# Kernel optimization log

Measured on AMD Instinct MI355X. Metric: run time of the kernel, lower is better.

## Reference

```python
import jax, jax.numpy as jnp
import numpy as np

B, N, F_IN, F_OUT, E = 8, 20000, 128, 128, 320000
ALPHA = 0.2  # LeakyReLU negative slope


def _xavier_normal(key, shape, gain=1.414):
    fan_in, fan_out = shape[0], shape[1]
    std = gain * np.sqrt(2.0 / (fan_in + fan_out))
    return jax.random.normal(key, shape, dtype=jnp.float32) * std


def setup_inputs() -> dict:
    key = jax.random.key(0)
    k1, k2, k3, k4, k5 = jax.random.split(key, 5)
    x = jax.random.normal(k1, (B, N, F_IN), dtype=jnp.float32)
    W = _xavier_normal(k2, (F_IN, F_OUT))
    a = _xavier_normal(k3, (2 * F_OUT, 1))
    # Edge list (src, dst). First N src are arange so every row has >=1 edge
    # (avoids div-by-zero in rowsum, matching a graph with no isolated sources).
    src_extra = jax.random.randint(k4, (E - N,), 0, N, dtype=jnp.int32)
    src = jnp.concatenate([jnp.arange(N, dtype=jnp.int32), src_extra])
    dst = jax.random.randint(k5, (E,), 0, N, dtype=jnp.int32)
    edge = jnp.stack([src, dst], axis=0)  # [2, E]
    return {"x": x, "W": W, "a": a, "edge": edge}


def reference(x, W, a, edge):
    # x: [B, N, F_in], W: [F_in, F_out], a: [2*F_out, 1], edge: [2, E]
    Fo = W.shape[1]
    n = x.shape[1]
    src, dst = edge[0], edge[1]
    h = jnp.einsum('bnf,fo->bno', x, W)  # [B, N, Fo]
    # cat(h[src], h[dst]) @ a  ==  (h @ a1)[src] + (h @ a2)[dst]
    a1, a2 = a[:Fo, 0], a[Fo:, 0]
    s = (h @ a1)[:, src] + (h @ a2)[:, dst]  # [B, E]
    score = jnp.where(s > 0, s, ALPHA * s)  # LeakyReLU
    e = jnp.exp(-score)  # [B, E]
    # spmm: h_prime[src] += e * h[dst]; rowsum[src] += e  (per batch)
    msg = e[..., None] * h[:, dst, :]  # [B, E, Fo]
    seg = jax.vmap(lambda m: jax.ops.segment_sum(m, src, num_segments=n))(msg)  # [B,N,Fo]
    rowsum = jax.vmap(lambda v: jax.ops.segment_sum(v, src, num_segments=n))(e)  # [B,N]
    h_prime = seg / rowsum[..., None]
    return jax.nn.elu(h_prime)  # concat=True -> ELU
```

## Files before the change

kernel.cpp:

```cpp
#include <hip/hip_runtime.h>

#define NB 8
#define NN 20000
#define FI 128
#define FO 128
#define NE 320000
#define ROWS (NB * NN)
#define LRALPHA 0.2f

typedef short bf16x8 __attribute__((ext_vector_type(8)));
typedef float f32x4 __attribute__((ext_vector_type(4)));

static __device__ __forceinline__ float b2f(unsigned short u) {
  return __uint_as_float(((unsigned int)u) << 16);
}
static __device__ __forceinline__ unsigned short f2b(float f) {
  unsigned int u = __float_as_uint(f);
  return (unsigned short)((u + 0x7FFFu + ((u >> 16) & 1u)) >> 16);
}

__global__ __launch_bounds__(256) void wt_kernel(const float* __restrict__ W,
                                                 unsigned short* __restrict__ Wb,
                                                 int* __restrict__ counts) {
  int idx = blockIdx.x * 256 + threadIdx.x;
  if (idx < FI * FO) {
    int k = idx >> 7, o = idx & 127;
    Wb[o * 128 + k] = f2b(W[idx]);
  }
  if (idx < NN) counts[idx] = 0;
}

#define LDW 136

__global__ __launch_bounds__(256) void gemm_kernel(
    const float* __restrict__ x, const unsigned short* __restrict__ Wb,
    const float* __restrict__ a,
    unsigned short* __restrict__ hb,
    float* __restrict__ g1, float* __restrict__ g2) {
  __shared__ __align__(16) unsigned short Ws[128 * LDW];
  const int tid = threadIdx.x;

  {
    const bf16x8* wsrc = (const bf16x8*)Wb;
#pragma unroll
    for (int it = 0; it < 8; ++it) {
      int c = tid + it * 256;
      int o = c >> 4, seg = c & 15;
      *(bf16x8*)&Ws[o * LDW + seg * 8] = wsrc[c];
    }
  }

  const int wv = tid >> 6;
  const int lane = tid & 63;
  const int m = lane & 15;
  const int quad = lane >> 4;
  const size_t row0 = (size_t)blockIdx.x * 64 + wv * 16;

  const float* xr = x + (row0 + m) * 128;
  bf16x8 afr[4];
#pragma unroll
  for (int k0 = 0; k0 < 4; ++k0) {
    const float4* xp = (const float4*)(xr + k0 * 32 + quad * 8);
    float4 v0 = xp[0];
    float4 v1 = xp[1];
    union { bf16x8 v; unsigned short u[8]; } af;
    af.u[0] = f2b(v0.x); af.u[1] = f2b(v0.y);
    af.u[2] = f2b(v0.z); af.u[3] = f2b(v0.w);
    af.u[4] = f2b(v1.x); af.u[5] = f2b(v1.y);
    af.u[6] = f2b(v1.z); af.u[7] = f2b(v1.w);
    afr[k0] = af.v;
  }
  __syncthreads();

  f32x4 acc[8] = {};
#pragma unroll
  for (int k0 = 0; k0 < 4; ++k0) {
#pragma unroll
    for (int c = 0; c < 8; ++c) {
      bf16x8 bf = *(const bf16x8*)&Ws[(c * 16 + m) * LDW + k0 * 32 + quad * 8];
      acc[c] = __builtin_amdgcn_mfma_f32_16x16x32_bf16(afr[k0], bf, acc[c], 0, 0, 0);
    }
  }

  unsigned short* hp = hb + row0 * 128;
#pragma unroll
  for (int c = 0; c < 8; ++c)
#pragma unroll
    for (int r = 0; r < 4; ++r)
      hp[(quad * 4 + r) * 128 + c * 16 + m] = f2b(acc[c][r]);

  float a1v[8], a2v[8];
#pragma unroll
  for (int c = 0; c < 8; ++c) {
    a1v[c] = a[c * 16 + m];
    a2v[c] = a[128 + c * 16 + m];
  }
  float p1[4] = {}, p2[4] = {};
#pragma unroll
  for (int c = 0; c < 8; ++c)
#pragma unroll
    for (int r = 0; r < 4; ++r) {
      p1[r] = fmaf(acc[c][r], a1v[c], p1[r]);
      p2[r] = fmaf(acc[c][r], a2v[c], p2[r]);
    }
#pragma unroll
  for (int off = 1; off < 16; off <<= 1)
#pragma unroll
    for (int r = 0; r < 4; ++r) {
      p1[r] += __shfl_xor(p1[r], off, 64);
      p2[r] += __shfl_xor(p2[r], off, 64);
    }
  if (m == 0) {
    size_t rbase = row0 + quad * 4;
#pragma unroll
    for (int r = 0; r < 4; ++r) {
      g1[rbase + r] = p1[r];
      g2[rbase + r] = p2[r];
    }
  }
}

__global__ __launch_bounds__(256) void hist_kernel(const int* __restrict__ src,
                                                   int* __restrict__ counts) {
  int e = blockIdx.x * 256 + threadIdx.x;
  if (e < NE) atomicAdd(&counts[src[e]], 1);
}

__global__ __launch_bounds__(1024) void scan_kernel(
    const int* __restrict__ counts, int* __restrict__ offsets,
    int* __restrict__ cursor) {
  __shared__ int sc[NN];
  __shared__ int sums[1024];
  const int t = threadIdx.x;
  for (int idx = t; idx < NN; idx += 1024) sc[idx] = counts[idx];
  __syncthreads();
  int local[20];
  int base = t * 20;
  int s = 0;
#pragma unroll
  for (int c = 0; c < 20; ++c) {
    int idx = base + c;
    int v = (idx < NN) ? sc[idx] : 0;
    local[c] = s;
    s += v;
  }
  sums[t] = s;
  __syncthreads();
  for (int off = 1; off < 1024; off <<= 1) {
    int u = 0;
    if (t >= off) u = sums[t - off];
    __syncthreads();
    sums[t] += u;
    __syncthreads();
  }
  int prefix = sums[t] - s;
#pragma unroll
  for (int c = 0; c < 20; ++c) {
    int idx = base + c;
    if (idx < NN) {
      int o = prefix + local[c];
      offsets[idx] = o;
      cursor[idx] = o;
    }
  }
  if (t == 0) offsets[NN] = NE;
}

__global__ __launch_bounds__(256) void scatter_kernel(
    const int* __restrict__ src, const int* __restrict__ dst,
    int* __restrict__ cursor, int* __restrict__ csr_dst) {
  int e = blockIdx.x * 256 + threadIdx.x;
  if (e < NE) {
    int s = src[e];
    int d = dst[e];
    int pos = atomicAdd(&cursor[s], 1);
    csr_dst[pos] = d;
  }
}

__global__ __launch_bounds__(64) void gather_kernel(
    const unsigned short* __restrict__ hb, const float* __restrict__ g1,
    const float* __restrict__ g2, const int* __restrict__ offsets,
    const int* __restrict__ csr_dst, float* __restrict__ out) {
  const int i = blockIdx.x;
  const int b = blockIdx.y;
  const int lane = threadIdx.x;
  const int quad = lane >> 4;
  const int beg = offsets[i];
  const int deg = offsets[i + 1] - beg;
  const float g1i = g1[(size_t)b * NN + i];
  const float* g2b = g2 + (size_t)b * NN;
  const char* hbase = (const char*)(hb + (size_t)b * NN * 128) + (lane & 15) * 16;

  float acc[8] = {};
  float rs = 0.f;
  for (int c0 = 0; c0 < deg; c0 += 64) {
    const int cnt = min(64, deg - c0);
    int myd = 0;
    float w = 0.f;
    if (lane < cnt) {
      myd = csr_dst[beg + c0 + lane];
      float s = g1i + g2b[myd];
      float sc = fmaxf(s, LRALPHA * s);
      w = __expf(-sc);
    }
    rs += w;
    const int cr = (cnt + 15) & ~15;
    for (int e = 0; e < cr; e += 16) {
      bf16x8 hv[4];
      float we[4];
#pragma unroll
      for (int j = 0; j < 4; ++j) {
        int idx = e + j * 4 + quad;
        int d = __shfl(myd, idx, 64);
        we[j] = __shfl(w, idx, 64);
        hv[j] = *(const bf16x8*)(hbase + (d << 8));
      }
#pragma unroll
      for (int j = 0; j < 4; ++j) {
        union { bf16x8 v; unsigned short u[8]; } hu;
        hu.v = hv[j];
#pragma unroll
        for (int k = 0; k < 8; ++k)
          acc[k] = fmaf(we[j], b2f(hu.u[k]), acc[k]);
      }
    }
  }
#pragma unroll
  for (int k = 0; k < 8; ++k) {
    acc[k] += __shfl_xor(acc[k], 16, 64);
    acc[k] += __shfl_xor(acc[k], 32, 64);
  }
#pragma unroll
  for (int off = 32; off >= 1; off >>= 1) rs += __shfl_xor(rs, off, 64);

  if (lane < 16) {
    float inv = 1.f / rs;
    float o[8];
#pragma unroll
    for (int k = 0; k < 8; ++k) {
      float v = acc[k] * inv;
      o[k] = v > 0.f ? v : expm1f(v);
    }
    float4* op = (float4*)(out + ((size_t)b * NN + i) * 128 + lane * 8);
    op[0] = make_float4(o[0], o[1], o[2], o[3]);
    op[1] = make_float4(o[4], o[5], o[6], o[7]);
  }
}

extern "C" void kernel_launch(void* const* d_in, const int* in_sizes, int n_in,
                              void* d_out, int out_size, void* d_ws, size_t ws_size,
                              hipStream_t stream) {
  const float* x = (const float*)d_in[0];
  const float* W = (const float*)d_in[1];
  const float* a = (const float*)d_in[2];
  const int* edge = (const int*)d_in[3];
  const int* src = edge;
  const int* dst = edge + NE;
  float* out = (float*)d_out;

  char* p = (char*)d_ws;
  unsigned short* hb = (unsigned short*)p;  p += (size_t)ROWS * 128 * 2;
  float* g1 = (float*)p;                    p += (size_t)ROWS * 4;
  float* g2 = (float*)p;                    p += (size_t)ROWS * 4;
  int* counts = (int*)p;                    p += (size_t)NN * 4;
  int* offsets = (int*)p;                   p += (size_t)(NN + 1) * 4;
  int* cursor = (int*)p;                    p += (size_t)NN * 4;
  int* csr_dst = (int*)p;                   p += (size_t)NE * 4;
  unsigned short* Wb = (unsigned short*)p;  p += (size_t)FI * FO * 2;

  wt_kernel<<<80, 256, 0, stream>>>(W, Wb, counts);
  gemm_kernel<<<ROWS / 64, 256, 0, stream>>>(x, Wb, a, hb, g1, g2);
  hist_kernel<<<(NE + 255) / 256, 256, 0, stream>>>(src, counts);
  scan_kernel<<<1, 1024, 0, stream>>>(counts, offsets, cursor);
  scatter_kernel<<<(NE + 255) / 256, 256, 0, stream>>>(src, dst, cursor, csr_dst);
  dim3 ggrid(NN, NB);
  gather_kernel<<<ggrid, 64, 0, stream>>>(hb, g1, g2, offsets, csr_dst, out);
}
```

Measured before the change: 294.4 us.

## Interleave batches in h layout and gather all batches per node in one wave

The gemm now writes h as node-major with the 8 batches interleaved, so one destination's features for all batches form a contiguous 2KB block, and writes g1/g2 in a matching layout. Edge weights for all 8 batches are computed once per edge in the scatter kernel and stored in CSR order. The gather kernel then handles one node across all batches per wave and reads each neighbour index once instead of eight times, with 16-wide index prefetch. This cuts repeated CSR and score traffic and improves the contiguity of the gathers, at the cost of an extra 10MB weight buffer and more registers per lane.

```diff
diff --git a/kernel.cpp b/kernel.cpp
--- a/kernel.cpp
+++ b/kernel.cpp
@@ -35,8 +35,8 @@
 __global__ __launch_bounds__(256) void gemm_kernel(
     const float* __restrict__ x, const unsigned short* __restrict__ Wb,
     const float* __restrict__ a,
-    unsigned short* __restrict__ hb,
-    float* __restrict__ g1, float* __restrict__ g2) {
+    unsigned short* __restrict__ hbT,
+    float* __restrict__ g1T, float* __restrict__ g2T) {
   __shared__ __align__(16) unsigned short Ws[128 * LDW];
   const int tid = threadIdx.x;
 
@@ -55,6 +55,8 @@
   const int m = lane & 15;
   const int quad = lane >> 4;
   const size_t row0 = (size_t)blockIdx.x * 64 + wv * 16;
+  const int b = (int)(row0 / NN);
+  const int n0 = (int)(row0 - (size_t)b * NN);
 
   const float* xr = x + (row0 + m) * 128;
   bf16x8 afr[4];
@@ -82,12 +84,12 @@
     }
   }
 
-  unsigned short* hp = hb + row0 * 128;
+  unsigned short* hp = hbT + ((size_t)n0 * 8 + b) * 128;
 #pragma unroll
   for (int c = 0; c < 8; ++c)
 #pragma unroll
     for (int r = 0; r < 4; ++r)
-      hp[(quad * 4 + r) * 128 + c * 16 + m] = f2b(acc[c][r]);
+      hp[(size_t)(quad * 4 + r) * 1024 + c * 16 + m] = f2b(acc[c][r]);
 
   float a1v[8], a2v[8];
 #pragma unroll
@@ -111,11 +113,11 @@
       p2[r] += __shfl_xor(p2[r], off, 64);
     }
   if (m == 0) {
-    size_t rbase = row0 + quad * 4;
+    int nb = n0 + quad * 4;
 #pragma unroll
     for (int r = 0; r < 4; ++r) {
-      g1[rbase + r] = p1[r];
-      g2[rbase + r] = p2[r];
+      g1T[(size_t)(nb + r) * 8 + b] = p1[r];
+      g2T[(size_t)(nb + r) * 8 + b] = p2[r];
     }
   }
 }
@@ -168,84 +170,108 @@
 
 __global__ __launch_bounds__(256) void scatter_kernel(
     const int* __restrict__ src, const int* __restrict__ dst,
-    int* __restrict__ cursor, int* __restrict__ csr_dst) {
+    int* __restrict__ cursor, int* __restrict__ csr_dst,
+    const float* __restrict__ g1T, const float* __restrict__ g2T,
+    float* __restrict__ wT) {
   int e = blockIdx.x * 256 + threadIdx.x;
   if (e < NE) {
     int s = src[e];
     int d = dst[e];
     int pos = atomicAdd(&cursor[s], 1);
     csr_dst[pos] = d;
-  }
-}
-
-__global__ __launch_bounds__(64) void gather_kernel(
-    const unsigned short* __restrict__ hb, const float* __restrict__ g1,
-    const float* __restrict__ g2, const int* __restrict__ offsets,
-    const int* __restrict__ csr_dst, float* __restrict__ out) {
-  const int i = blockIdx.x;
-  const int b = blockIdx.y;
-  const int lane = threadIdx.x;
-  const int quad = lane >> 4;
+    const float4* g1p = (const float4*)(g1T + (size_t)s * 8);
+    const float4* g2p = (const float4*)(g2T + (size_t)d * 8);
+    float4 sa = g1p[0], sb = g1p[1];
+    float4 da = g2p[0], db = g2p[1];
+    float sv[8] = {sa.x + da.x, sa.y + da.y, sa.z + da.z, sa.w + da.w,
+                   sb.x + db.x, sb.y + db.y, sb.z + db.z, sb.w + db.w};
+    float w[8];
+#pragma unroll
+    for (int bi = 0; bi < 8; ++bi) {
+      float sc = fmaxf(sv[bi], LRALPHA * sv[bi]);
+      w[bi] = __expf(-sc);
+    }
+    float4* wp = (float4*)(wT + (size_t)pos * 8);
+    wp[0] = make_float4(w[0], w[1], w[2], w[3]);
+    wp[1] = make_float4(w[4], w[5], w[6], w[7]);
+  }
+}
+
+__global__ __launch_bounds__(256) void gather_kernel(
+    const unsigned short* __restrict__ hbT, const float* __restrict__ wT,
+    const int* __restrict__ offsets, const int* __restrict__ csr_dst,
+    float* __restrict__ out) {
+  const int i = blockIdx.x * 4 + (threadIdx.x >> 6);
+  const int lane = threadIdx.x & 63;
+  const int bq = lane >> 3;
+  const int sl = lane & 7;
   const int beg = offsets[i];
   const int deg = offsets[i + 1] - beg;
-  const float g1i = g1[(size_t)b * NN + i];
-  const float* g2b = g2 + (size_t)b * NN;
-  const char* hbase = (const char*)(hb + (size_t)b * NN * 128) + (lane & 15) * 16;
-
-  float acc[8] = {};
+  const char* hl = (const char*)hbT + (size_t)lane * 32;
+  const float* wl = wT + bq;
+
+  float acc[16] = {};
   float rs = 0.f;
-  for (int c0 = 0; c0 < deg; c0 += 64) {
-    const int cnt = min(64, deg - c0);
-    int myd = 0;
-    float w = 0.f;
-    if (lane < cnt) {
-      myd = csr_dst[beg + c0 + lane];
-      float s = g1i + g2b[myd];
-      float sc = fmaxf(s, LRALPHA * s);
-      w = __expf(-sc);
-    }
-    rs += w;
-    const int cr = (cnt + 15) & ~15;
-    for (int e = 0; e < cr; e += 16) {
-      bf16x8 hv[4];
-      float we[4];
+  int c0 = 0;
+  int dvec = csr_dst[beg + min(lane & 15, deg - 1)];
+
+  for (; c0 + 16 <= deg; c0 += 16) {
+    int dnext = csr_dst[beg + min(c0 + 16 + (lane & 15), deg - 1)];
+#pragma unroll
+    for (int j = 0; j < 16; ++j) {
+      int d = __shfl(dvec, j, 16);
+      float w = wl[(size_t)(beg + c0 + j) * 8];
+      const char* hp = hl + ((size_t)d << 11);
+      bf16x8 h0 = *(const bf16x8*)hp;
+      bf16x8 h1 = *(const bf16x8*)(hp + 16);
+      rs += w;
+      union { bf16x8 v; unsigned short u[8]; } a0, a1;
+      a0.v = h0; a1.v = h1;
+#pragma unroll
+      for (int k = 0; k < 8; ++k) {
+        acc[k]     = fmaf(w, b2f(a0.u[k]), acc[k]);
+        acc[8 + k] = fmaf(w, b2f(a1.u[k]), acc[8 + k]);
+      }
+    }
+    dvec = dnext;
+  }
+  {
+    const int lim = deg - c0;
+    for (int t = 0; t < lim; t += 4) {
 #pragma unroll
       for (int j = 0; j < 4; ++j) {
-        int idx = e + j * 4 + quad;
-        int d = __shfl(myd, idx, 64);
-        we[j] = __shfl(w, idx, 64);
-        hv[j] = *(const bf16x8*)(hbase + (d << 8));
+        int u = t + j;
+        bool v = u < lim;
+        int d = __shfl(dvec, v ? u : (lim - 1), 16);
+        float w = v ? wl[(size_t)(beg + c0 + u) * 8] : 0.f;
+        const char* hp = hl + ((size_t)d << 11);
+        bf16x8 h0 = *(const bf16x8*)hp;
+        bf16x8 h1 = *(const bf16x8*)(hp + 16);
+        rs += w;
+        union { bf16x8 v; unsigned short u8[8]; } a0, a1;
+        a0.v = h0; a1.v = h1;
+#pragma unroll
+        for (int k = 0; k < 8; ++k) {
+          acc[k]     = fmaf(w, b2f(a0.u8[k]), acc[k]);
+          acc[8 + k] = fmaf(w, b2f(a1.u8[k]), acc[8 + k]);
+        }
       }
-#pragma unroll
-      for (int j = 0; j < 4; ++j) {
-        union { bf16x8 v; unsigned short u[8]; } hu;
-        hu.v = hv[j];
-#pragma unroll
-        for (int k = 0; k < 8; ++k)
-          acc[k] = fmaf(we[j], b2f(hu.u[k]), acc[k]);
-      }
-    }
-  }
-#pragma unroll
-  for (int k = 0; k < 8; ++k) {
-    acc[k] += __shfl_xor(acc[k], 16, 64);
-    acc[k] += __shfl_xor(acc[k], 32, 64);
-  }
-#pragma unroll
-  for (int off = 32; off >= 1; off >>= 1) rs += __shfl_xor(rs, off, 64);
-
-  if (lane < 16) {
-    float inv = 1.f / rs;
-    float o[8];
-#pragma unroll
-    for (int k = 0; k < 8; ++k) {
-      float v = acc[k] * inv;
-      o[k] = v > 0.f ? v : expm1f(v);
-    }
-    float4* op = (float4*)(out + ((size_t)b * NN + i) * 128 + lane * 8);
-    op[0] = make_float4(o[0], o[1], o[2], o[3]);
-    op[1] = make_float4(o[4], o[5], o[6], o[7]);
-  }
+    }
+  }
+
+  float inv = 1.f / rs;
+  float o[16];
+#pragma unroll
+  for (int k = 0; k < 16; ++k) {
+    float v = acc[k] * inv;
+    o[k] = v > 0.f ? v : expm1f(v);
+  }
+  float* op = out + ((size_t)bq * NN + i) * 128 + sl * 16;
+  float4* op4 = (float4*)op;
+  op4[0] = make_float4(o[0], o[1], o[2], o[3]);
+  op4[1] = make_float4(o[4], o[5], o[6], o[7]);
+  op4[2] = make_float4(o[8], o[9], o[10], o[11]);
+  op4[3] = make_float4(o[12], o[13], o[14], o[15]);
 }
 
 extern "C" void kernel_launch(void* const* d_in, const int* in_sizes, int n_in,
@@ -260,20 +286,21 @@
   float* out = (float*)d_out;
 
   char* p = (char*)d_ws;
-  unsigned short* hb = (unsigned short*)p;  p += (size_t)ROWS * 128 * 2;
-  float* g1 = (float*)p;                    p += (size_t)ROWS * 4;
-  float* g2 = (float*)p;                    p += (size_t)ROWS * 4;
+  unsigned short* hbT = (unsigned short*)p; p += (size_t)ROWS * 128 * 2;
+  float* g1T = (float*)p;                   p += (size_t)ROWS * 4;
+  float* g2T = (float*)p;                   p += (size_t)ROWS * 4;
   int* counts = (int*)p;                    p += (size_t)NN * 4;
   int* offsets = (int*)p;                   p += (size_t)(NN + 1) * 4;
   int* cursor = (int*)p;                    p += (size_t)NN * 4;
   int* csr_dst = (int*)p;                   p += (size_t)NE * 4;
+  float* wT = (float*)p;                    p += (size_t)NE * 8 * 4;
   unsigned short* Wb = (unsigned short*)p;  p += (size_t)FI * FO * 2;
 
   wt_kernel<<<80, 256, 0, stream>>>(W, Wb, counts);
-  gemm_kernel<<<ROWS / 64, 256, 0, stream>>>(x, Wb, a, hb, g1, g2);
+  gemm_kernel<<<ROWS / 64, 256, 0, stream>>>(x, Wb, a, hbT, g1T, g2T);
   hist_kernel<<<(NE + 255) / 256, 256, 0, stream>>>(src, counts);
   scan_kernel<<<1, 1024, 0, stream>>>(counts, offsets, cursor);
-  scatter_kernel<<<(NE + 255) / 256, 256, 0, stream>>>(src, dst, cursor, csr_dst);
-  dim3 ggrid(NN, NB);
-  gather_kernel<<<ggrid, 64, 0, stream>>>(hb, g1, g2, offsets, csr_dst, out);
-}
+  scatter_kernel<<<(NE + 255) / 256, 256, 0, stream>>>(src, dst, cursor, csr_dst,
+                                                       g1T, g2T, wT);
+  gather_kernel<<<NN / 4, 256, 0, stream>>>(hbT, wT, offsets, csr_dst, out);
+}
```

Measured after the change: 310.7 us. 5.5% more time.
